# Performance work log

Measured on AMD Instinct MI355X. Metric: run time of the kernel, lower is better.

## Reference

```python
import jax, jax.numpy as jnp
import numpy as np
import math

NUM_HEADS = 16

def _skew(QEr):
    # QEr: [B, H, S, S] -> pad 1 on left of last dim, reshape, drop first row
    B, H, S, _ = QEr.shape
    padded = jnp.pad(QEr, ((0, 0), (0, 0), (0, 0), (1, 0)))  # [B,H,S,S+1]
    reshaped = padded.reshape(B, H, S + 1, S)
    return reshaped[:, :, 1:, :]  # [B,H,S,S]

def setup_inputs() -> dict:
    key = jax.random.key(0)
    ks = jax.random.split(key, 8)
    B, S, D, dh = 4, 1024, 1024, 64
    x = jax.random.normal(ks[0], (B, S, D), dtype=jnp.float32)
    scale = 1.0 / math.sqrt(D)
    Wq = jax.random.normal(ks[1], (D, D), dtype=jnp.float32) * scale
    Wk = jax.random.normal(ks[2], (D, D), dtype=jnp.float32) * scale
    Wv = jax.random.normal(ks[3], (D, D), dtype=jnp.float32) * scale
    bq = jnp.zeros((D,), dtype=jnp.float32)
    bk = jnp.zeros((D,), dtype=jnp.float32)
    bv = jnp.zeros((D,), dtype=jnp.float32)
    Er = jax.random.normal(ks[4], (S, dh), dtype=jnp.float32)
    return {"x": x, "Wq": Wq, "bq": bq, "Wk": Wk, "bk": bk, "Wv": Wv, "bv": bv, "Er": Er}

def reference(x, Wq, bq, Wk, bk, Wv, bv, Er):
    B, S, D = x.shape
    H = NUM_HEADS
    dh = D // H
    # Linear projections (torch Linear: x @ W.T + b)
    q = (x @ Wq.T + bq).reshape(B, S, H, dh).transpose(0, 2, 1, 3)  # [B,H,S,dh]
    k = (x @ Wk.T + bk).reshape(B, S, H, dh).transpose(0, 2, 1, 3)
    v = (x @ Wv.T + bv).reshape(B, S, H, dh).transpose(0, 2, 1, 3)
    # Relative position term: q @ Er^T then skew (start = max_len - S = 0)
    QEr = jnp.einsum('bhsd,td->bhst', q, Er)  # [B,H,S,S]
    Srel = _skew(QEr)
    QKt = jnp.einsum('bhsd,bhtd->bhst', q, k)  # [B,H,S,S]
    attn = (QKt + Srel) / math.sqrt(dh)
    causal = jnp.tril(jnp.ones((S, S), dtype=bool))
    attn = jnp.where(causal[None, None], attn, jnp.float32(-1e6))
    attn = jax.nn.softmax(attn, axis=-1)
    out = jnp.einsum('bhst,bhtd->bhsd', attn, v)  # [B,H,S,dh]
    out = out.transpose(0, 2, 1, 3).reshape(B, S, D)
    return out  # dropout is identity in eval / p=0
```

## Files before the change

kernel.cpp:

```cpp
#include <hip/hip_runtime.h>
#include <stdint.h>

#define S_LEN 1024
#define DM 1024
#define NH 16
#define DH 64
#define NB 4

typedef unsigned short u16;
typedef __attribute__((ext_vector_type(8))) short short8;
typedef __attribute__((ext_vector_type(4))) float f32x4;
typedef __attribute__((ext_vector_type(4))) unsigned int u32x4;

__device__ __forceinline__ u16 f2bf(float f) {
  union { float f; unsigned int u; } c;
  c.f = f;
  unsigned int u = c.u;
  return (u16)((u + 0x7fffu + ((u >> 16) & 1u)) >> 16);
}

__device__ __forceinline__ void g2l16(const void* g, void* l) {
  __builtin_amdgcn_global_load_lds(
      (const __attribute__((address_space(1))) unsigned int*)(uintptr_t)g,
      (__attribute__((address_space(3))) unsigned int*)(uint32_t)(uintptr_t)l,
      16, 0, 0);
}

__device__ __forceinline__ float grp16_max(float v) {
  union { float f; int i; } c, o;
  c.f = v; o.i = __builtin_amdgcn_update_dpp(c.i, c.i, 0xB1, 0xF, 0xF, false);
  v = fmaxf(v, o.f);
  c.f = v; o.i = __builtin_amdgcn_update_dpp(c.i, c.i, 0x4E, 0xF, 0xF, false);
  v = fmaxf(v, o.f);
  c.f = v; o.i = __builtin_amdgcn_update_dpp(c.i, c.i, 0x124, 0xF, 0xF, false);
  v = fmaxf(v, o.f);
  c.f = v; o.i = __builtin_amdgcn_update_dpp(c.i, c.i, 0x128, 0xF, 0xF, false);
  v = fmaxf(v, o.f);
  return v;
}
__device__ __forceinline__ float grp16_sum(float v) {
  union { float f; int i; } c, o;
  c.f = v; o.i = __builtin_amdgcn_update_dpp(c.i, c.i, 0xB1, 0xF, 0xF, false);
  v += o.f;
  c.f = v; o.i = __builtin_amdgcn_update_dpp(c.i, c.i, 0x4E, 0xF, 0xF, false);
  v += o.f;
  c.f = v; o.i = __builtin_amdgcn_update_dpp(c.i, c.i, 0x124, 0xF, 0xF, false);
  v += o.f;
  c.f = v; o.i = __builtin_amdgcn_update_dpp(c.i, c.i, 0x128, 0xF, 0xF, false);
  v += o.f;
  return v;
}

__global__ __launch_bounds__(256) void cvt_f32_bf16(
    const float* __restrict__ x, const float* __restrict__ Wq,
    const float* __restrict__ Wk, const float* __restrict__ Wv,
    const float* __restrict__ Er, u16* __restrict__ xb,
    u16* __restrict__ Wqb, u16* __restrict__ Wkb, u16* __restrict__ Wvb,
    u16* __restrict__ Erb) {
  const size_t f = ((size_t)blockIdx.x * 256 + threadIdx.x) * 8;
  const float* src;
  u16* dst;
  size_t off;
  if (f < 4194304) { src = x; dst = xb; off = f; }
  else if (f < 5242880) { src = Wq; dst = Wqb; off = f - 4194304; }
  else if (f < 6291456) { src = Wk; dst = Wkb; off = f - 5242880; }
  else if (f < 7340032) { src = Wv; dst = Wvb; off = f - 6291456; }
  else { src = Er; dst = Erb; off = f - 7340032; }
  const float4 a = *(const float4*)(src + off);
  const float4 b = *(const float4*)(src + off + 4);
  u16 o[8] = {f2bf(a.x), f2bf(a.y), f2bf(a.z), f2bf(a.w),
              f2bf(b.x), f2bf(b.y), f2bf(b.z), f2bf(b.w)};
  *(u32x4*)(dst + off) = *(const u32x4*)o;
}

__global__ __launch_bounds__(256) void qkv_gemm(
    const u16* __restrict__ x,
    const u16* __restrict__ Wq, const float* __restrict__ bq,
    const u16* __restrict__ Wk, const float* __restrict__ bk,
    const u16* __restrict__ Wv, const float* __restrict__ bv,
    u16* __restrict__ Qo, u16* __restrict__ Ko, u16* __restrict__ Vo) {
  __shared__ __attribute__((aligned(16))) u16 Al[128 * 32];
  __shared__ __attribute__((aligned(16))) u16 Bl[128 * 32];

  const int tid = threadIdx.x;
  const int lane = tid & 63;
  const int wave = tid >> 6;
  const int z = blockIdx.z;
  const u16* W = (z == 0) ? Wq : (z == 1) ? Wk : Wv;
  const float* bias = (z == 0) ? bq : (z == 1) ? bk : bv;

  const int m0 = blockIdx.y * 128;
  const int n0 = blockIdx.x * 128;

  f32x4 acc[4][4];
  const f32x4 fzero = {0.f, 0.f, 0.f, 0.f};
#pragma unroll
  for (int i = 0; i < 4; i++)
#pragma unroll
    for (int j = 0; j < 4; j++) acc[i][j] = fzero;

  const int srow = tid >> 2;
  const int schunk = tid & 3;
  const u16* gA = x + (size_t)(m0 + srow) * DM + schunk * 8;
  const u16* gB = W + (size_t)(n0 + srow) * DM + schunk * 8;

  const int fr = lane & 15;
  const int fq = lane >> 4;
  const int wr = (wave >> 1) * 64;
  const int wc = (wave & 1) * 64;

  for (int k = 0; k < DM; k += 32) {
    g2l16(gA + k, &Al[tid * 8]);
    g2l16(gA + (size_t)64 * DM + k, &Al[2048 + tid * 8]);
    g2l16(gB + k, &Bl[tid * 8]);
    g2l16(gB + (size_t)64 * DM + k, &Bl[2048 + tid * 8]);
    __syncthreads();
    short8 a[4], b[4];
#pragma unroll
    for (int i = 0; i < 4; i++)
      a[i] = *(const short8*)&Al[(wr + i * 16 + fr) * 32 + fq * 8];
#pragma unroll
    for (int j = 0; j < 4; j++)
      b[j] = *(const short8*)&Bl[(wc + j * 16 + fr) * 32 + fq * 8];
#pragma unroll
    for (int i = 0; i < 4; i++)
#pragma unroll
      for (int j = 0; j < 4; j++)
        acc[i][j] =
            __builtin_amdgcn_mfma_f32_16x16x32_bf16(a[i], b[j], acc[i][j], 0, 0, 0);
    __syncthreads();
  }

#pragma unroll
  for (int j = 0; j < 4; j++) {
    const int n = n0 + wc + j * 16 + fr;
    const float bsv = bias[n];
    const int h = n >> 6, d = n & (DH - 1);
#pragma unroll
    for (int i = 0; i < 4; i++) {
#pragma unroll
      for (int r = 0; r < 4; r++) {
        const int m = m0 + wr + i * 16 + fq * 4 + r;
        const int bb = m >> 10, s = m & (S_LEN - 1);
        const u16 o = f2bf(acc[i][j][r] + bsv);
        if (z == 2)
          Vo[((size_t)(bb * NH + h) * DH + d) * S_LEN + s] = o;
        else if (z == 1)
          Ko[((size_t)(bb * NH + h) * S_LEN + s) * DH + d] = o;
        else
          Qo[((size_t)(bb * NH + h) * S_LEN + s) * DH + d] = o;
      }
    }
  }
}

__global__ __launch_bounds__(256, 4) void attn(
    const u16* __restrict__ Q, const u16* __restrict__ K,
    const u16* __restrict__ Vt, const u16* __restrict__ Er,
    float* __restrict__ out) {
  __shared__ __attribute__((aligned(16))) u16 Kl[64 * 64];
  __shared__ __attribute__((aligned(16))) u16 Vl[64 * 64];
  __shared__ __attribute__((aligned(16))) u16 El[128 * 64];
  __shared__ __attribute__((aligned(16))) u16 Pl[4][16 * 64];

  const int tid = threadIdx.x;
  const int lane = tid & 63;
  const int w = tid >> 6;
  const int bh = blockIdx.y;
  const int b = bh >> 4, h = bh & (NH - 1);
  const int it = ((int)blockIdx.x + bh + ((bh >> 4) << 2)) & 15;
  const int i0 = it * 64;
  const int i0w = i0 + w * 16;
  const int E0b = S_LEN - 64 - i0;

  const u16* Qb = Q + (size_t)bh * S_LEN * DH;
  const char* Kb = (const char*)(K + (size_t)bh * S_LEN * DH);
  const char* Vb = (const char*)(Vt + (size_t)bh * DH * S_LEN);
  const char* Eb = (const char*)Er;
  u16* Pw = Pl[w];

  const int fr = lane & 15;
  const int fq = lane >> 4;
  const f32x4 fzero = {0.f, 0.f, 0.f, 0.f};

  const int r8 = tid >> 3;
  const int ch = (tid & 7) * 16;

  auto stageKV = [&](int j0) {
#pragma unroll
    for (int p = 0; p < 2; p++) {
      const int row = p * 32 + r8;
      const int sw = ch ^ ((row & 7) << 4);
      g2l16(Kb + (size_t)(j0 + row) * 128 + sw, (char*)Kl + row * 128 + ch);
      g2l16(Vb + (size_t)row * 2048 + j0 * 2 + sw, (char*)Vl + row * 128 + ch);
    }
  };
  auto stageEl = [&](int e0, int np) {
    for (int p = 0; p < np; p++) {
      const int e = e0 + p * 32 + r8;
      const int slot = e & 127;
      const int ec = (e > S_LEN - 1) ? (S_LEN - 1) : e;
      const int sw = ch ^ ((slot & 7) << 4);
      g2l16(Eb + (size_t)ec * 128 + sw, (char*)El + slot * 128 + ch);
    }
  };

  const short8 aq0 = *(const short8*)&Qb[(size_t)(i0w + fr) * DH + fq * 8];
  const short8 aq1 = *(const short8*)&Qb[(size_t)(i0w + fr) * DH + 32 + fq * 8];

  float mrow[4], lrow[4];
  f32x4 accO[4];
#pragma unroll
  for (int r = 0; r < 4; r++) { mrow[r] = -3.0e38f; lrow[r] = 0.f; }
#pragma unroll
  for (int t = 0; t < 4; t++) accO[t] = fzero;

  f32x4 zzc = fzero;
  const int ksw = (fr & 7) << 4;

  for (int j0 = 0; j0 <= i0; j0 += 64) {
    stageKV(j0);
    if (j0 == 0) stageEl(E0b, 4);
    else stageEl(E0b + j0 + 64, 2);
    __syncthreads();

    int tmax = (i0w + 15 - j0) >> 4;
    if (tmax > 3) tmax = 3;

    f32x4 sfr[4];
#pragma unroll
    for (int t = 0; t < 4; t++) sfr[t] = fzero;
    __builtin_amdgcn_s_setprio(1);
#pragma unroll
    for (int t = 0; t < 4; t++)
      if (t <= tmax) {
        const char* kr = (const char*)Kl + (t * 16 + fr) * 128;
        const short8 b0 = *(const short8*)(kr + ((fq * 16) ^ ksw));
        const short8 b1 = *(const short8*)(kr + ((64 + fq * 16) ^ ksw));
        f32x4 z = fzero;
        z = __builtin_amdgcn_mfma_f32_16x16x32_bf16(aq0, b0, z, 0, 0, 0);
        z = __builtin_amdgcn_mfma_f32_16x16x32_bf16(aq1, b1, z, 0, 0, 0);
        sfr[t] = z;
      }
    __builtin_amdgcn_s_setprio(0);

    const int ebs = S_LEN - 16 - i0w + j0;
    f32x4 zz[5];
#pragma unroll
    for (int f = 0; f < 5; f++) zz[f] = fzero;
    const int f0 = (j0 == 0) ? 0 : 1;
#pragma unroll
    for (int f = 0; f < 5; f++)
      if (f >= f0 && f <= tmax + 1) {
        const int slot = ((ebs + f * 16) & 127) + fr;
        const char* er = (const char*)El + slot * 128;
        const short8 b0 = *(const short8*)(er + ((fq * 16) ^ ksw));
        const short8 b1 = *(const short8*)(er + ((64 + fq * 16) ^ ksw));
        f32x4 z = fzero;
        z = __builtin_amdgcn_mfma_f32_16x16x32_bf16(aq0, b0, z, 0, 0, 0);
        z = __builtin_amdgcn_mfma_f32_16x16x32_bf16(aq1, b1, z, 0, 0, 0);
        zz[f] = z;
      }
    if (j0 > 0) zz[0] = zzc;
    zzc = zz[4];

    float p[4][4];
#pragma unroll
    for (int r = 0; r < 4; r++) {
      const int row = fq * 4 + r;
      const int c = 15 - row + fr;
      const int src = (fq << 4) | (c & 15);
      float sh[5];
#pragma unroll
      for (int f = 0; f < 5; f++) sh[f] = __shfl(zz[f][r], src);
#pragma unroll
      for (int t = 0; t < 4; t++) {
        const float rel = (c < 16) ? sh[t] : sh[t + 1];
        float sv = (sfr[t][r] + rel) * 0.125f;
        const int jj = j0 + t * 16 + fr;
        const int ii = i0w + row;
        if (jj > ii) sv = -3.0e38f;
        p[t][r] = sv;
      }
    }

#pragma unroll
    for (int r = 0; r < 4; r++) {
      float rm = fmaxf(fmaxf(p[0][r], p[1][r]), fmaxf(p[2][r], p[3][r]));
      rm = grp16_max(rm);
      const float mnew = fmaxf(mrow[r], rm);
      const float alpha = __expf(mrow[r] - mnew);
      mrow[r] = mnew;
      float rs = 0.f;
#pragma unroll
      for (int t = 0; t < 4; t++) {
        const float e = __expf(p[t][r] - mnew);
        p[t][r] = e;
        rs += e;
      }
      rs = grp16_sum(rs);
      lrow[r] = lrow[r] * alpha + rs;
#pragma unroll
      for (int t = 0; t < 4; t++) accO[t][r] *= alpha;
    }

#pragma unroll
    for (int t = 0; t < 4; t++)
#pragma unroll
      for (int r = 0; r < 4; r++)
        Pw[(fq * 4 + r) * 64 + (((t ^ fq) << 4) + fr)] = f2bf(p[t][r]);
    __builtin_amdgcn_s_waitcnt(0xC07F);

    const int rsw = (fr >> 2) << 4;
    const short8 ap0 = *(const short8*)&Pw[fr * 64 + ((fq * 8) ^ rsw)];
    const short8 ap1 = *(const short8*)&Pw[fr * 64 + ((32 + fq * 8) ^ rsw)];

    __builtin_amdgcn_s_setprio(1);
#pragma unroll
    for (int t = 0; t < 4; t++) {
      const char* vr = (const char*)Vl + (t * 16 + fr) * 128;
      const short8 b0 = *(const short8*)(vr + ((fq * 16) ^ ksw));
      const short8 b1 = *(const short8*)(vr + ((64 + fq * 16) ^ ksw));
      accO[t] =
          __builtin_amdgcn_mfma_f32_16x16x32_bf16(ap0, b0, accO[t], 0, 0, 0);
      accO[t] =
          __builtin_amdgcn_mfma_f32_16x16x32_bf16(ap1, b1, accO[t], 0, 0, 0);
    }
    __builtin_amdgcn_s_setprio(0);

    __syncthreads();
  }

#pragma unroll
  for (int r = 0; r < 4; r++) {
    const float inv = 1.f / lrow[r];
    const int s = i0w + fq * 4 + r;
#pragma unroll
    for (int t = 0; t < 4; t++) {
      const int d = t * 16 + fr;
      out[((size_t)b * S_LEN + s) * DM + h * DH + d] = accO[t][r] * inv;
    }
  }
}

extern "C" void kernel_launch(void* const* d_in, const int* in_sizes, int n_in,
                              void* d_out, int out_size, void* d_ws, size_t ws_size,
                              hipStream_t stream) {
  const float* x = (const float*)d_in[0];
  const float* Wq = (const float*)d_in[1];
  const float* bq = (const float*)d_in[2];
  const float* Wk = (const float*)d_in[3];
  const float* bk = (const float*)d_in[4];
  const float* Wv = (const float*)d_in[5];
  const float* bv = (const float*)d_in[6];
  const float* Er = (const float*)d_in[7];
  float* out = (float*)d_out;

  const size_t per = (size_t)NB * NH * S_LEN * DH;
  u16* Qw = (u16*)d_ws;
  u16* Kw = Qw + per;
  u16* Vw = Kw + per;
  u16* xb = Vw + per;
  u16* Wqb = xb + per;
  u16* Wkb = Wqb + (size_t)DM * DM;
  u16* Wvb = Wkb + (size_t)DM * DM;
  u16* Erb = Wvb + (size_t)DM * DM;

  cvt_f32_bf16<<<3616, 256, 0, stream>>>(x, Wq, Wk, Wv, Er, xb, Wqb, Wkb, Wvb,
                                         Erb);
  dim3 g1(DM / 128, (NB * S_LEN) / 128, 3);
  qkv_gemm<<<g1, dim3(256), 0, stream>>>(xb, Wqb, bq, Wkb, bk, Wvb, bv, Qw, Kw,
                                         Vw);
  dim3 g2(16, NB * NH);
  attn<<<g2, dim3(256), 0, stream>>>(Qw, Kw, Vw, Erb, out);
}
```

Baseline: 174.9 us.

## Double-buffer QKV GEMM, vectorize stores, lazy softmax rescale with exp2

The QKV GEMM now double-buffers its LDS tiles, so the next K-slice loads while the current one computes, and it drops one barrier per iteration. Q/K use swapped MFMA operands so each lane holds four consecutive columns and can issue vectorized 4-wide bf16 stores, and V stores are vectorized as well. In attention, the scale folds log2(e) so the kernel can use the native exp2. Row-max rescaling is skipped when every row's new max stays within a threshold of the running max, and the per-row sum reduction is deferred to the end. The lazy rescale relies on the exponent bound to avoid overflow, and it adds a wave-wide vote per tile.

Measured after the change: 231.0 us. 1.32x slower.

```diff
diff --git a/kernel.cpp b/kernel.cpp
--- a/kernel.cpp
+++ b/kernel.cpp
@@ -11,6 +11,9 @@
 typedef __attribute__((ext_vector_type(8))) short short8;
 typedef __attribute__((ext_vector_type(4))) float f32x4;
 typedef __attribute__((ext_vector_type(4))) unsigned int u32x4;
+typedef __attribute__((ext_vector_type(4))) unsigned short u16x4;
+
+#define SCL 0.18033688011112042f
 
 __device__ __forceinline__ u16 f2bf(float f) {
   union { float f; unsigned int u; } c;
@@ -79,8 +82,8 @@
     const u16* __restrict__ Wk, const float* __restrict__ bk,
     const u16* __restrict__ Wv, const float* __restrict__ bv,
     u16* __restrict__ Qo, u16* __restrict__ Ko, u16* __restrict__ Vo) {
-  __shared__ __attribute__((aligned(16))) u16 Al[128 * 32];
-  __shared__ __attribute__((aligned(16))) u16 Bl[128 * 32];
+  __shared__ __attribute__((aligned(16))) u16 Al[2][128 * 32];
+  __shared__ __attribute__((aligned(16))) u16 Bl[2][128 * 32];
 
   const int tid = threadIdx.x;
   const int lane = tid & 63;
@@ -109,46 +112,78 @@
   const int wr = (wave >> 1) * 64;
   const int wc = (wave & 1) * 64;
 
+  auto stageAB = [&](int k, int bf) {
+    g2l16(gA + k, &Al[bf][tid * 8]);
+    g2l16(gA + (size_t)64 * DM + k, &Al[bf][2048 + tid * 8]);
+    g2l16(gB + k, &Bl[bf][tid * 8]);
+    g2l16(gB + (size_t)64 * DM + k, &Bl[bf][2048 + tid * 8]);
+  };
+
+  stageAB(0, 0);
+  __syncthreads();
+  int bf = 0;
+
   for (int k = 0; k < DM; k += 32) {
-    g2l16(gA + k, &Al[tid * 8]);
-    g2l16(gA + (size_t)64 * DM + k, &Al[2048 + tid * 8]);
-    g2l16(gB + k, &Bl[tid * 8]);
-    g2l16(gB + (size_t)64 * DM + k, &Bl[2048 + tid * 8]);
+    if (k + 32 < DM) stageAB(k + 32, bf ^ 1);
+    short8 a[4], b[4];
+#pragma unroll
+    for (int i = 0; i < 4; i++)
+      a[i] = *(const short8*)&Al[bf][(wr + i * 16 + fr) * 32 + fq * 8];
+#pragma unroll
+    for (int j = 0; j < 4; j++)
+      b[j] = *(const short8*)&Bl[bf][(wc + j * 16 + fr) * 32 + fq * 8];
+    if (z == 2) {
+#pragma unroll
+      for (int i = 0; i < 4; i++)
+#pragma unroll
+        for (int j = 0; j < 4; j++)
+          acc[i][j] = __builtin_amdgcn_mfma_f32_16x16x32_bf16(a[i], b[j],
+                                                              acc[i][j], 0, 0, 0);
+    } else {
+#pragma unroll
+      for (int i = 0; i < 4; i++)
+#pragma unroll
+        for (int j = 0; j < 4; j++)
+          acc[i][j] = __builtin_amdgcn_mfma_f32_16x16x32_bf16(b[j], a[i],
+                                                              acc[i][j], 0, 0, 0);
+    }
     __syncthreads();
-    short8 a[4], b[4];
-#pragma unroll
-    for (int i = 0; i < 4; i++)
-      a[i] = *(const short8*)&Al[(wr + i * 16 + fr) * 32 + fq * 8];
-#pragma unroll
-    for (int j = 0; j < 4; j++)
-      b[j] = *(const short8*)&Bl[(wc + j * 16 + fr) * 32 + fq * 8];
-#pragma unroll
-    for (int i = 0; i < 4; i++)
-#pragma unroll
-      for (int j = 0; j < 4; j++)
-        acc[i][j] =
-            __builtin_amdgcn_mfma_f32_16x16x32_bf16(a[i], b[j], acc[i][j], 0, 0, 0);
-    __syncthreads();
+    bf ^= 1;
   }
 
-#pragma unroll
-  for (int j = 0; j < 4; j++) {
-    const int n = n0 + wc + j * 16 + fr;
-    const float bsv = bias[n];
-    const int h = n >> 6, d = n & (DH - 1);
+  if (z == 2) {
+#pragma unroll
+    for (int j = 0; j < 4; j++) {
+      const int n = n0 + wc + j * 16 + fr;
+      const float bsv = bias[n];
+      const int h = n >> 6, d = n & (DH - 1);
+#pragma unroll
+      for (int i = 0; i < 4; i++) {
+        const int mb = m0 + wr + i * 16 + fq * 4;
+        const int bb = mb >> 10, s = mb & (S_LEN - 1);
+        u16x4 o;
+#pragma unroll
+        for (int r = 0; r < 4; r++) o[r] = f2bf(acc[i][j][r] + bsv);
+        *(u16x4*)&Vo[((size_t)(bb * NH + h) * DH + d) * S_LEN + s] = o;
+      }
+    }
+  } else {
+    u16* O = (z == 0) ? Qo : Ko;
 #pragma unroll
     for (int i = 0; i < 4; i++) {
-#pragma unroll
-      for (int r = 0; r < 4; r++) {
-        const int m = m0 + wr + i * 16 + fq * 4 + r;
-        const int bb = m >> 10, s = m & (S_LEN - 1);
-        const u16 o = f2bf(acc[i][j][r] + bsv);
-        if (z == 2)
-          Vo[((size_t)(bb * NH + h) * DH + d) * S_LEN + s] = o;
-        else if (z == 1)
-          Ko[((size_t)(bb * NH + h) * S_LEN + s) * DH + d] = o;
-        else
-          Qo[((size_t)(bb * NH + h) * S_LEN + s) * DH + d] = o;
+      const int m = m0 + wr + i * 16 + fr;
+      const int bb = m >> 10, s = m & (S_LEN - 1);
+#pragma unroll
+      for (int j = 0; j < 4; j++) {
+        const int nb = n0 + wc + j * 16 + fq * 4;
+        const float4 b4 = *(const float4*)&bias[nb];
+        const int h = nb >> 6, d = nb & (DH - 1);
+        u16x4 o;
+        o[0] = f2bf(acc[i][j][0] + b4.x);
+        o[1] = f2bf(acc[i][j][1] + b4.y);
+        o[2] = f2bf(acc[i][j][2] + b4.z);
+        o[3] = f2bf(acc[i][j][3] + b4.w);
+        *(u16x4*)&O[((size_t)(bb * NH + h) * S_LEN + s) * DH + d] = o;
       }
     }
   }
@@ -208,10 +243,10 @@
   const short8 aq0 = *(const short8*)&Qb[(size_t)(i0w + fr) * DH + fq * 8];
   const short8 aq1 = *(const short8*)&Qb[(size_t)(i0w + fr) * DH + 32 + fq * 8];
 
-  float mrow[4], lrow[4];
+  float mrow[4], lp[4];
   f32x4 accO[4];
 #pragma unroll
-  for (int r = 0; r < 4; r++) { mrow[r] = -3.0e38f; lrow[r] = 0.f; }
+  for (int r = 0; r < 4; r++) { mrow[r] = -3.0e38f; lp[r] = 0.f; }
 #pragma unroll
   for (int t = 0; t < 4; t++) accO[t] = fzero;
 
@@ -276,7 +311,7 @@
 #pragma unroll
       for (int t = 0; t < 4; t++) {
         const float rel = (c < 16) ? sh[t] : sh[t + 1];
-        float sv = (sfr[t][r] + rel) * 0.125f;
+        float sv = (sfr[t][r] + rel) * SCL;
         const int jj = j0 + t * 16 + fr;
         const int ii = i0w + row;
         if (jj > ii) sv = -3.0e38f;
@@ -284,24 +319,44 @@
       }
     }
 
+    float rm4[4];
+    int small = 1;
 #pragma unroll
     for (int r = 0; r < 4; r++) {
       float rm = fmaxf(fmaxf(p[0][r], p[1][r]), fmaxf(p[2][r], p[3][r]));
       rm = grp16_max(rm);
-      const float mnew = fmaxf(mrow[r], rm);
-      const float alpha = __expf(mrow[r] - mnew);
-      mrow[r] = mnew;
-      float rs = 0.f;
-#pragma unroll
-      for (int t = 0; t < 4; t++) {
-        const float e = __expf(p[t][r] - mnew);
-        p[t][r] = e;
-        rs += e;
-      }
-      rs = grp16_sum(rs);
-      lrow[r] = lrow[r] * alpha + rs;
-#pragma unroll
-      for (int t = 0; t < 4; t++) accO[t][r] *= alpha;
+      rm4[r] = rm;
+      small &= (rm <= mrow[r] + 11.0f) ? 1 : 0;
+    }
+    if (__all(small)) {
+#pragma unroll
+      for (int r = 0; r < 4; r++) {
+        float rs = 0.f;
+#pragma unroll
+        for (int t = 0; t < 4; t++) {
+          const float e = __builtin_amdgcn_exp2f(p[t][r] - mrow[r]);
+          p[t][r] = e;
+          rs += e;
+        }
+        lp[r] += rs;
+      }
+    } else {
+#pragma unroll
+      for (int r = 0; r < 4; r++) {
+        const float mnew = fmaxf(mrow[r], rm4[r]);
+        const float alpha = __builtin_amdgcn_exp2f(mrow[r] - mnew);
+        mrow[r] = mnew;
+        float rs = 0.f;
+#pragma unroll
+        for (int t = 0; t < 4; t++) {
+          const float e = __builtin_amdgcn_exp2f(p[t][r] - mnew);
+          p[t][r] = e;
+          rs += e;
+        }
+        lp[r] = lp[r] * alpha + rs;
+#pragma unroll
+        for (int t = 0; t < 4; t++) accO[t][r] *= alpha;
+      }
     }
 
 #pragma unroll
@@ -333,7 +388,8 @@
 
 #pragma unroll
   for (int r = 0; r < 4; r++) {
-    const float inv = 1.f / lrow[r];
+    const float lr = grp16_sum(lp[r]);
+    const float inv = 1.f / lr;
     const int s = i0w + fq * 4 + r;
 #pragma unroll
     for (int t = 0; t < 4; t++) {
```
